# Kernel tuning notes

Measured on AMD Instinct MI355X. Metric: run time of the kernel, lower is better.

The kernel has to match this reference:

```python
import jax, jax.numpy as jnp
import numpy as np

NUM_HEADS = 12

def _get_rel_pos(size, rel_pos):
    # q_size == k_size == size, no interpolation needed (table has 2*size-1 rows)
    idx = jnp.arange(size)[:, None] - jnp.arange(size)[None, :] + (size - 1)  # (size,size)
    return rel_pos[idx]  # (size, size, head_dim)

def setup_inputs() -> dict:
    key = jax.random.key(0)
    ks = jax.random.split(key, 7)
    B, H, W, dim = 8, 32, 32, 768
    head_dim = dim // NUM_HEADS
    return {
        "x": jax.random.normal(ks[0], (B, H, W, dim), jnp.float32),
        "qkv_w": jax.random.normal(ks[1], (dim, 3 * dim), jnp.float32) * 0.02,
        "qkv_b": jax.random.normal(ks[2], (3 * dim,), jnp.float32) * 0.02,
        "proj_w": jax.random.normal(ks[3], (dim, dim), jnp.float32) * 0.02,
        "proj_b": jax.random.normal(ks[4], (dim,), jnp.float32) * 0.02,
        "rel_pos_h": jax.random.normal(ks[5], (2 * H - 1, head_dim), jnp.float32) * 0.02,
        "rel_pos_w": jax.random.normal(ks[6], (2 * W - 1, head_dim), jnp.float32) * 0.02,
    }

def reference(x, qkv_w, qkv_b, proj_w, proj_b, rel_pos_h, rel_pos_w):
    B, H, W, dim = x.shape
    N = H * W
    head_dim = dim // NUM_HEADS
    scale = head_dim ** (-0.5)

    qkv = x.reshape(B, N, dim) @ qkv_w + qkv_b                     # (B,N,3*dim)
    qkv = qkv.reshape(B, N, 3, NUM_HEADS, head_dim)
    qkv = qkv.transpose(2, 0, 3, 1, 4).reshape(3, B * NUM_HEADS, N, head_dim)
    q, k, v = qkv[0], qkv[1], qkv[2]                               # (B*h, N, hd)

    attn = jnp.einsum("bnd,bmd->bnm", q * scale, k)                # (B*h, N, N)

    # decomposed relative position bias
    Rh = _get_rel_pos(H, rel_pos_h)                                # (H,H,hd)
    Rw = _get_rel_pos(W, rel_pos_w)                                # (W,W,hd)
    r_q = q.reshape(B * NUM_HEADS, H, W, head_dim)
    rel_h = jnp.einsum("bhwc,hkc->bhwk", r_q, Rh)                  # (B*h,H,W,H)
    rel_w = jnp.einsum("bhwc,wkc->bhwk", r_q, Rw)                  # (B*h,H,W,W)
    attn = (attn.reshape(B * NUM_HEADS, H, W, H, W)
            + rel_h[:, :, :, :, None]
            + rel_w[:, :, :, None, :]).reshape(B * NUM_HEADS, N, N)

    attn = jax.nn.softmax(attn, axis=-1)
    out = jnp.einsum("bnm,bmd->bnd", attn, v)                      # (B*h, N, hd)
    out = out.reshape(B, NUM_HEADS, H, W, head_dim).transpose(0, 2, 3, 1, 4).reshape(B, H, W, dim)
    return out @ proj_w + proj_b
```

## Files before the change

kernel.cpp:

```cpp
#include <hip/hip_runtime.h>
#include <hip/hip_bf16.h>
#include <math.h>

#define DIM   768
#define NHEAD 12
#define NQ    1024

typedef short  short8  __attribute__((ext_vector_type(8)));
typedef unsigned short us8 __attribute__((ext_vector_type(8)));
typedef float  f32x16  __attribute__((ext_vector_type(16)));

#if __has_builtin(__builtin_amdgcn_exp2f)
#define EXP2(x) __builtin_amdgcn_exp2f(x)
#else
#define EXP2(x) __expf(0.69314718056f * (x))
#endif
#define LOG2E 1.44269504089f

__device__ inline ushort f2b(float f) {
  union { float f; unsigned u; } c; c.f = f;
  unsigned r = (c.u + 0x7FFFu + ((c.u >> 16) & 1u)) >> 16;
  return (ushort)r;
}
__device__ inline float b2f(ushort h) {
  union { unsigned u; float f; } c; c.u = ((unsigned)h) << 16;
  return c.f;
}
__device__ inline ushort4 cvt4(float4 v) {
  ushort4 o; o.x = f2b(v.x); o.y = f2b(v.y); o.z = f2b(v.z); o.w = f2b(v.w);
  return o;
}
__device__ inline unsigned pkf(float a, float b) {
  return (unsigned)f2b(a) | ((unsigned)f2b(b) << 16);
}

__global__ __launch_bounds__(256) void prep(
    const float* __restrict__ x, const float* __restrict__ qkv_w,
    const float* __restrict__ proj_w, ushort* __restrict__ Xb,
    ushort* __restrict__ Wqt, ushort* __restrict__ Wpt) {
  __shared__ ushort Ts[64][68];
  const int blk = blockIdx.x, tid = threadIdx.x;
  if (blk < 768) {
    const float4* src = (const float4*)x;
    ushort4* dst = (ushort4*)Xb;
    int base = blk * 2048;
#pragma unroll
    for (int it = 0; it < 8; ++it) {
      int i = base + it * 256 + tid;
      dst[i] = cvt4(src[i]);
    }
    return;
  }
  const float* W; ushort* Wt; int ncols, tk, tn;
  if (blk < 1200) { int t = blk - 768;  W = qkv_w; Wt = Wqt; ncols = 2304; tk = t % 12; tn = t / 12; }
  else            { int t = blk - 1200; W = proj_w; Wt = Wpt; ncols = 768; tk = t % 12; tn = t / 12; }
  const int kb = tk * 64, nb = tn * 64;
#pragma unroll
  for (int rr = 0; rr < 4; ++rr) {
    int r = (tid >> 4) + rr * 16, c4 = (tid & 15) * 4;
    float4 w = *(const float4*)(W + (size_t)(kb + r) * ncols + nb + c4);
    *(ushort4*)&Ts[r][c4] = cvt4(w);
  }
  __syncthreads();
#pragma unroll
  for (int wwi = 0; wwi < 2; ++wwi) {
    int n = (tid >> 3) + wwi * 32, k8 = (tid & 7) * 8;
    us8 v;
#pragma unroll
    for (int j = 0; j < 8; ++j) v[j] = Ts[k8 + j][n];
    *(us8*)(Wt + (size_t)(nb + n) * 768 + kb + k8) = v;
  }
}

template <int OUTBF>
__global__ __launch_bounds__(256, 2) void gemm_mfma(
    const ushort* __restrict__ A, const ushort* __restrict__ BT,
    const float* __restrict__ bias, void* __restrict__ Cp, int Nc) {
  __shared__ ushort Asl[128][72];
  __shared__ ushort Bsl[128][72];
  const int tid = threadIdx.x;
  const int bm = blockIdx.y * 128, bn = blockIdx.x * 128;
  const int lane = tid & 63, wv = tid >> 6;
  const int l31 = lane & 31, lh = lane >> 5;
  const int wm = (wv >> 1) * 64, wn = (wv & 1) * 64;

  f32x16 acc[2][2];
#pragma unroll
  for (int i = 0; i < 2; ++i)
#pragma unroll
    for (int j = 0; j < 2; ++j)
#pragma unroll
      for (int r = 0; r < 16; ++r) acc[i][j][r] = 0.f;

  for (int kt = 0; kt < 768; kt += 64) {
    __syncthreads();
#pragma unroll
    for (int it = 0; it < 4; ++it) {
      int item = tid + 256 * it;
      int r = item >> 3, c8 = (item & 7) * 8;
      *(us8*)&Asl[r][c8] = *(const us8*)(A + (size_t)(bm + r) * 768 + kt + c8);
      *(us8*)&Bsl[r][c8] = *(const us8*)(BT + (size_t)(bn + r) * 768 + kt + c8);
    }
    __syncthreads();
#pragma unroll
    for (int ks = 0; ks < 4; ++ks) {
      short8 a0 = *(const short8*)&Asl[wm + l31][ks * 16 + lh * 8];
      short8 a1 = *(const short8*)&Asl[wm + 32 + l31][ks * 16 + lh * 8];
      short8 b0 = *(const short8*)&Bsl[wn + l31][ks * 16 + lh * 8];
      short8 b1 = *(const short8*)&Bsl[wn + 32 + l31][ks * 16 + lh * 8];
      acc[0][0] = __builtin_amdgcn_mfma_f32_32x32x16_bf16(a0, b0, acc[0][0], 0, 0, 0);
      acc[0][1] = __builtin_amdgcn_mfma_f32_32x32x16_bf16(a0, b1, acc[0][1], 0, 0, 0);
      acc[1][0] = __builtin_amdgcn_mfma_f32_32x32x16_bf16(a1, b0, acc[1][0], 0, 0, 0);
      acc[1][1] = __builtin_amdgcn_mfma_f32_32x32x16_bf16(a1, b1, acc[1][1], 0, 0, 0);
    }
  }

#pragma unroll
  for (int mb = 0; mb < 2; ++mb)
#pragma unroll
    for (int nb = 0; nb < 2; ++nb) {
      int col = bn + wn + nb * 32 + l31;
      float bv = bias[col];
#pragma unroll
      for (int reg = 0; reg < 16; ++reg) {
        int row = bm + wm + mb * 32 + (reg & 3) + 8 * (reg >> 2) + 4 * lh;
        float o = acc[mb][nb][reg] + bv;
        if (OUTBF) ((ushort*)Cp)[(size_t)row * Nc + col] = f2b(o);
        else       ((float*)Cp)[(size_t)row * Nc + col] = o;
      }
    }
}

__global__ __launch_bounds__(256) void bias_kernel(
    const ushort* __restrict__ QKV, const float* __restrict__ rph,
    const float* __restrict__ rpw, ushort* __restrict__ RH,
    ushort* __restrict__ RW) {
  __shared__ ushort Qb[128][72];
  __shared__ ushort Tb[63][72];

  const int tid = threadIdx.x;
  const int bh = blockIdx.x;
  const int gy = blockIdx.y;
  const int b = bh / NHEAD, h = bh % NHEAD;
  const bool isH = gy < 8;
  const int g4 = isH ? gy : (gy - 8);
  const int lane = tid & 63, wv = tid >> 6;
  const int l31 = lane & 31, lh = lane >> 5;

  const ushort* qb = QKV + (size_t)b * NQ * 2304 + h * 64;
  const float* tab = isH ? rph : rpw;

#pragma unroll
  for (int it = 0; it < 4; ++it) {
    int item = tid + 256 * it;
    if (item < 63 * 16) {
      int r = item >> 4, q4 = (item & 15) * 4;
      float4 v = *(const float4*)(tab + r * 64 + q4);
      *(ushort4*)&Tb[r][q4] = cvt4(v);
    }
  }
#pragma unroll
  for (int it = 0; it < 4; ++it) {
    int item = tid + 256 * it;
    int r = item >> 3, c8 = (item & 7) * 8;
    int n = isH ? (g4 * 128 + r) : ((r & 31) * 32 + g4 * 4 + (r >> 5));
    *(us8*)&Qb[r][c8] = *(const us8*)(qb + (size_t)n * 2304 + c8);
  }
  __syncthreads();

  const int fixed = g4 * 4 + wv;
  f32x16 acc;
#pragma unroll
  for (int i = 0; i < 16; ++i) acc[i] = 0.f;
#pragma unroll
  for (int ks = 0; ks < 4; ++ks) {
    short8 a  = *(const short8*)&Qb[wv * 32 + l31][ks * 16 + lh * 8];
    short8 bb = *(const short8*)&Tb[fixed + 31 - l31][ks * 16 + lh * 8];
    acc = __builtin_amdgcn_mfma_f32_32x32x16_bf16(a, bb, acc, 0, 0, 0);
  }
  ushort* outp = isH ? RH : RW;
#pragma unroll
  for (int reg = 0; reg < 16; ++reg) {
    int row = (reg & 3) + 8 * (reg >> 2) + 4 * lh;
    int n = isH ? (fixed * 32 + row) : (row * 32 + fixed);
    outp[((size_t)bh * NQ + n) * 32 + l31] = f2b(acc[reg] * LOG2E);
  }
}

__global__ __launch_bounds__(256, 3) void attn_mfma(
    const ushort* __restrict__ QKV, const ushort* __restrict__ RH,
    const ushort* __restrict__ RW, ushort* __restrict__ O) {
  __shared__ ushort Qs[128][72];
  __shared__ ushort Ks[64][72];
  __shared__ ushort VT[64][72];

  const int tid = threadIdx.x;
  const int bh = blockIdx.x % 96;
  const int qt = blockIdx.x / 96;
  const int b = bh / NHEAD, h = bh % NHEAD;
  const int n0 = qt * 128;
  const int lane = tid & 63, wv = tid >> 6;
  const int l31 = lane & 31, lh = lane >> 5;
  const int wb = wv * 32;

  const ushort* qb = QKV + (size_t)b * NQ * 2304 + h * 64;
  const ushort* kb = qb + DIM;
  const ushort* vb = qb + 2 * DIM;

#pragma unroll
  for (int it = 0; it < 4; ++it) {
    int item = tid + 256 * it;
    int r = item >> 3, c8 = (item & 7) * 8;
    *(us8*)&Qs[r][c8] = *(const us8*)(qb + (size_t)(n0 + r) * 2304 + c8);
  }

  const int q = n0 + wb + l31;
  const ushort* rwrow = RW + ((size_t)bh * NQ + q) * 32;
  float rwv[16];
#pragma unroll
  for (int g = 0; g < 4; ++g) {
    ushort4 v = *(const ushort4*)(rwrow + 8 * g + 4 * lh);
    rwv[4 * g + 0] = b2f(v.x); rwv[4 * g + 1] = b2f(v.y);
    rwv[4 * g + 2] = b2f(v.z); rwv[4 * g + 3] = b2f(v.w);
  }
  const ushort* rhrow = RH + ((size_t)bh * NQ + q) * 32;

  __syncthreads();
  short8 aq[4];
#pragma unroll
  for (int ks = 0; ks < 4; ++ks)
    aq[ks] = *(const short8*)&Qs[wb + l31][ks * 16 + lh * 8];

  ushort* Pb2 = &Qs[0][0] + wv * (32 * 40);

  f32x16 oacc0, oacc1;
#pragma unroll
  for (int i = 0; i < 16; ++i) { oacc0[i] = 0.f; oacc1[i] = 0.f; }
  float lacc = 0.f;

  for (int t = 0; t < 16; ++t) {
    const int kt = t * 64;
    __syncthreads();
    const unsigned rhu = *(const unsigned*)(rhrow + 2 * t);
#pragma unroll
    for (int it = 0; it < 2; ++it) {
      int item = tid + 256 * it;
      int r = item >> 3, c8 = (item & 7) * 8;
      *(us8*)&Ks[r][c8] = *(const us8*)(kb + (size_t)(kt + r) * 2304 + c8);
    }
#pragma unroll
    for (int it = 0; it < 2; ++it) {
      int item = tid + 256 * it;
      int p = item & 31, d4 = (item >> 5) * 4;
      ushort4 v0 = *(const ushort4*)(vb + (size_t)(kt + 2 * p) * 2304 + d4);
      ushort4 v1 = *(const ushort4*)(vb + (size_t)(kt + 2 * p + 1) * 2304 + d4);
      *(unsigned*)&VT[d4 + 0][2 * p] = (unsigned)v0.x | ((unsigned)v1.x << 16);
      *(unsigned*)&VT[d4 + 1][2 * p] = (unsigned)v0.y | ((unsigned)v1.y << 16);
      *(unsigned*)&VT[d4 + 2][2 * p] = (unsigned)v0.z | ((unsigned)v1.z << 16);
      *(unsigned*)&VT[d4 + 3][2 * p] = (unsigned)v0.w | ((unsigned)v1.w << 16);
    }
    __syncthreads();

    const float rh0 = b2f((ushort)(rhu & 0xFFFF));
    const float rh1 = b2f((ushort)(rhu >> 16));

#pragma unroll
    for (int cb = 0; cb < 2; ++cb) {
      f32x16 s;
#pragma unroll
      for (int i = 0; i < 16; ++i) s[i] = 0.f;
#pragma unroll
      for (int ks = 0; ks < 4; ++ks) {
        short8 ak = *(const short8*)&Ks[cb * 32 + l31][ks * 16 + lh * 8];
        s = __builtin_amdgcn_mfma_f32_32x32x16_bf16(ak, aq[ks], s, 0, 0, 0);
      }
      const float rhv = cb ? rh1 : rh0;
#pragma unroll
      for (int g = 0; g < 4; ++g) {
        float p0 = EXP2(fmaf(s[4 * g + 0], 0.18033688f, rwv[4 * g + 0] + rhv));
        float p1 = EXP2(fmaf(s[4 * g + 1], 0.18033688f, rwv[4 * g + 1] + rhv));
        float p2 = EXP2(fmaf(s[4 * g + 2], 0.18033688f, rwv[4 * g + 2] + rhv));
        float p3 = EXP2(fmaf(s[4 * g + 3], 0.18033688f, rwv[4 * g + 3] + rhv));
        lacc += (p0 + p1) + (p2 + p3);
        uint2 pk; pk.x = pkf(p0, p1); pk.y = pkf(p2, p3);
        *(uint2*)&Pb2[l31 * 40 + 8 * g + 4 * lh] = pk;
      }
#pragma unroll
      for (int ks = 0; ks < 2; ++ks) {
        short8 ap  = *(const short8*)&Pb2[l31 * 40 + ks * 16 + lh * 8];
        short8 bv0 = *(const short8*)&VT[l31][cb * 32 + ks * 16 + lh * 8];
        short8 bv1 = *(const short8*)&VT[32 + l31][cb * 32 + ks * 16 + lh * 8];
        oacc0 = __builtin_amdgcn_mfma_f32_32x32x16_bf16(ap, bv0, oacc0, 0, 0, 0);
        oacc1 = __builtin_amdgcn_mfma_f32_32x32x16_bf16(ap, bv1, oacc1, 0, 0, 0);
      }
    }
  }

  lacc += __shfl_xor(lacc, 32);
  const float linv = 1.0f / lacc;
  ushort* ob = O + ((size_t)b * NQ + n0 + wb) * DIM + h * 64;
#pragma unroll
  for (int reg = 0; reg < 16; ++reg) {
    int row = (reg & 3) + 8 * (reg >> 2) + 4 * lh;
    float lq = __shfl(linv, row);
    ob[(size_t)row * DIM + l31]      = f2b(oacc0[reg] * lq);
    ob[(size_t)row * DIM + 32 + l31] = f2b(oacc1[reg] * lq);
  }
}

extern "C" void kernel_launch(void* const* d_in, const int* in_sizes, int n_in,
                              void* d_out, int out_size, void* d_ws, size_t ws_size,
                              hipStream_t stream) {
  const float* x      = (const float*)d_in[0];
  const float* qkv_w  = (const float*)d_in[1];
  const float* qkv_b  = (const float*)d_in[2];
  const float* proj_w = (const float*)d_in[3];
  const float* proj_b = (const float*)d_in[4];
  const float* rel_h  = (const float*)d_in[5];
  const float* rel_w  = (const float*)d_in[6];
  float* out = (float*)d_out;

  ushort* qkvb = (ushort*)d_ws;
  ushort* obuf = qkvb + (size_t)8192 * 2304;
  ushort* RH   = obuf + (size_t)8192 * DIM;
  ushort* RW   = RH + (size_t)96 * NQ * 32;
  ushort* Xb   = RW + (size_t)96 * NQ * 32;
  ushort* Wqt  = Xb + (size_t)8192 * DIM;
  ushort* Wpt  = Wqt + (size_t)2304 * DIM;

  prep<<<dim3(1344), 256, 0, stream>>>(x, qkv_w, proj_w, Xb, Wqt, Wpt);

  gemm_mfma<1><<<dim3(2304 / 128, 8192 / 128), 256, 0, stream>>>(
      Xb, Wqt, qkv_b, qkvb, 2304);

  bias_kernel<<<dim3(96, 16), 256, 0, stream>>>(qkvb, rel_h, rel_w, RH, RW);

  attn_mfma<<<dim3(96 * 8), 256, 0, stream>>>(qkvb, RH, RW, obuf);

  gemm_mfma<0><<<dim3(768 / 128, 8192 / 128), 256, 0, stream>>>(
      obuf, Wpt, proj_b, out, 768);
}
```

Before: 228.1 us.

## Write V transposed from QKV GEMM epilogue and simplify attention V loads

The QKV GEMM epilogue now writes the V columns straight into a per-head transposed buffer laid out as (b,h,d,n). The attention kernel can then load V^T tiles with contiguous 16-byte loads instead of strided gathers plus an in-register transpose. The P packing switches from round-to-nearest-even to a cheaper round-half-up using a byte permute, and the GEMM launch bound occupancy hint rises from 2 to 3 blocks. Costs are extra workspace, a scattered epilogue store pattern for V, and slightly different bf16 rounding of the probabilities.

```diff
diff --git a/kernel.cpp b/kernel.cpp
--- a/kernel.cpp
+++ b/kernel.cpp
@@ -30,8 +30,9 @@
   ushort4 o; o.x = f2b(v.x); o.y = f2b(v.y); o.z = f2b(v.z); o.w = f2b(v.w);
   return o;
 }
-__device__ inline unsigned pkf(float a, float b) {
-  return (unsigned)f2b(a) | ((unsigned)f2b(b) << 16);
+__device__ inline unsigned pkr(float a, float b) {
+  union { float f; unsigned u; } ca, cb; ca.f = a; cb.f = b;
+  return __builtin_amdgcn_perm(cb.u + 0x8000u, ca.u + 0x8000u, 0x07060302u);
 }
 
 __global__ __launch_bounds__(256) void prep(
@@ -73,9 +74,10 @@
 }
 
 template <int OUTBF>
-__global__ __launch_bounds__(256, 2) void gemm_mfma(
+__global__ __launch_bounds__(256, 3) void gemm_mfma(
     const ushort* __restrict__ A, const ushort* __restrict__ BT,
-    const float* __restrict__ bias, void* __restrict__ Cp, int Nc) {
+    const float* __restrict__ bias, void* __restrict__ Cp, int Nc,
+    ushort* __restrict__ VTg) {
   __shared__ ushort Asl[128][72];
   __shared__ ushort Bsl[128][72];
   const int tid = threadIdx.x;
@@ -115,20 +117,46 @@
     }
   }
 
-#pragma unroll
-  for (int mb = 0; mb < 2; ++mb)
+  const bool vreg = OUTBF && (bn >= 1536);
+  if (!vreg) {
+#pragma unroll
+    for (int mb = 0; mb < 2; ++mb)
+#pragma unroll
+      for (int nb = 0; nb < 2; ++nb) {
+        int col = bn + wn + nb * 32 + l31;
+        float bv = bias[col];
+#pragma unroll
+        for (int reg = 0; reg < 16; ++reg) {
+          int row = bm + wm + mb * 32 + (reg & 3) + 8 * (reg >> 2) + 4 * lh;
+          float o = acc[mb][nb][reg] + bv;
+          if (OUTBF) ((ushort*)Cp)[(size_t)row * Nc + col] = f2b(o);
+          else       ((float*)Cp)[(size_t)row * Nc + col] = o;
+        }
+      }
+  } else {
+    const int b_ = bm >> 10;
+    const int nbase = (bm & 1023) + wm;
 #pragma unroll
     for (int nb = 0; nb < 2; ++nb) {
       int col = bn + wn + nb * 32 + l31;
       float bv = bias[col];
-#pragma unroll
-      for (int reg = 0; reg < 16; ++reg) {
-        int row = bm + wm + mb * 32 + (reg & 3) + 8 * (reg >> 2) + 4 * lh;
-        float o = acc[mb][nb][reg] + bv;
-        if (OUTBF) ((ushort*)Cp)[(size_t)row * Nc + col] = f2b(o);
-        else       ((float*)Cp)[(size_t)row * Nc + col] = o;
-      }
-    }
+      int hd_ = col - 1536;
+      int h_ = hd_ >> 6, d_ = hd_ & 63;
+      ushort* vrow = VTg + ((size_t)(b_ * NHEAD + h_) * 64 + d_) * NQ;
+#pragma unroll
+      for (int mb = 0; mb < 2; ++mb)
+#pragma unroll
+        for (int g = 0; g < 4; ++g) {
+          int n = nbase + mb * 32 + 8 * g + 4 * lh;
+          ushort4 st;
+          st.x = f2b(acc[mb][nb][4 * g + 0] + bv);
+          st.y = f2b(acc[mb][nb][4 * g + 1] + bv);
+          st.z = f2b(acc[mb][nb][4 * g + 2] + bv);
+          st.w = f2b(acc[mb][nb][4 * g + 3] + bv);
+          *(ushort4*)(vrow + n) = st;
+        }
+    }
+  }
 }
 
 __global__ __launch_bounds__(256) void bias_kernel(
@@ -188,8 +216,9 @@
 }
 
 __global__ __launch_bounds__(256, 3) void attn_mfma(
-    const ushort* __restrict__ QKV, const ushort* __restrict__ RH,
-    const ushort* __restrict__ RW, ushort* __restrict__ O) {
+    const ushort* __restrict__ QKV, const ushort* __restrict__ VTg,
+    const ushort* __restrict__ RH, const ushort* __restrict__ RW,
+    ushort* __restrict__ O) {
   __shared__ ushort Qs[128][72];
   __shared__ ushort Ks[64][72];
   __shared__ ushort VT[64][72];
@@ -205,7 +234,7 @@
 
   const ushort* qb = QKV + (size_t)b * NQ * 2304 + h * 64;
   const ushort* kb = qb + DIM;
-  const ushort* vb = qb + 2 * DIM;
+  const ushort* vtg = VTg + (size_t)bh * 64 * NQ;
 
 #pragma unroll
   for (int it = 0; it < 4; ++it) {
@@ -251,13 +280,8 @@
 #pragma unroll
     for (int it = 0; it < 2; ++it) {
       int item = tid + 256 * it;
-      int p = item & 31, d4 = (item >> 5) * 4;
-      ushort4 v0 = *(const ushort4*)(vb + (size_t)(kt + 2 * p) * 2304 + d4);
-      ushort4 v1 = *(const ushort4*)(vb + (size_t)(kt + 2 * p + 1) * 2304 + d4);
-      *(unsigned*)&VT[d4 + 0][2 * p] = (unsigned)v0.x | ((unsigned)v1.x << 16);
-      *(unsigned*)&VT[d4 + 1][2 * p] = (unsigned)v0.y | ((unsigned)v1.y << 16);
-      *(unsigned*)&VT[d4 + 2][2 * p] = (unsigned)v0.z | ((unsigned)v1.z << 16);
-      *(unsigned*)&VT[d4 + 3][2 * p] = (unsigned)v0.w | ((unsigned)v1.w << 16);
+      int d = item >> 3, j8 = (item & 7) * 8;
+      *(us8*)&VT[d][j8] = *(const us8*)(vtg + (size_t)d * NQ + kt + j8);
     }
     __syncthreads();
 
@@ -282,7 +306,7 @@
         float p2 = EXP2(fmaf(s[4 * g + 2], 0.18033688f, rwv[4 * g + 2] + rhv));
         float p3 = EXP2(fmaf(s[4 * g + 3], 0.18033688f, rwv[4 * g + 3] + rhv));
         lacc += (p0 + p1) + (p2 + p3);
-        uint2 pk; pk.x = pkf(p0, p1); pk.y = pkf(p2, p3);
+        uint2 pk; pk.x = pkr(p0, p1); pk.y = pkr(p2, p3);
         *(uint2*)&Pb2[l31 * 40 + 8 * g + 4 * lh] = pk;
       }
 #pragma unroll
@@ -327,16 +351,17 @@
   ushort* Xb   = RW + (size_t)96 * NQ * 32;
   ushort* Wqt  = Xb + (size_t)8192 * DIM;
   ushort* Wpt  = Wqt + (size_t)2304 * DIM;
+  ushort* VTg  = Wpt + (size_t)DIM * DIM;
 
   prep<<<dim3(1344), 256, 0, stream>>>(x, qkv_w, proj_w, Xb, Wqt, Wpt);
 
   gemm_mfma<1><<<dim3(2304 / 128, 8192 / 128), 256, 0, stream>>>(
-      Xb, Wqt, qkv_b, qkvb, 2304);
+      Xb, Wqt, qkv_b, qkvb, 2304, VTg);
 
   bias_kernel<<<dim3(96, 16), 256, 0, stream>>>(qkvb, rel_h, rel_w, RH, RW);
 
-  attn_mfma<<<dim3(96 * 8), 256, 0, stream>>>(qkvb, RH, RW, obuf);
+  attn_mfma<<<dim3(96 * 8), 256, 0, stream>>>(qkvb, VTg, RH, RW, obuf);
 
   gemm_mfma<0><<<dim3(768 / 128, 8192 / 128), 256, 0, stream>>>(
-      obuf, Wpt, proj_b, out, 768);
-}
+      obuf, Wpt, proj_b, out, 768, nullptr);
+}
```

Measured after the change: 216.3 us. -5.2%, faster.
